# Kernel optimization log

Hardware: AMD Instinct MI355X
Metric: run time of the kernel (lower is better)

Reference implementation:

```python
import jax, jax.numpy as jnp
import numpy as np

S = 1        # support_num
K = 20       # neighbor_num for conv stages
EPS_BN = 1e-5

def _normalize(x, axis):
    n = jnp.linalg.norm(x, axis=axis, keepdims=True)
    return x / jnp.maximum(n, 1e-12)

def _knn(verts, k):
    # verts: (b, v, 3) -> (b, v, k) nearest-neighbor indices excluding self
    sq = jnp.sum(verts * verts, axis=-1)                                   # (b, v)
    d = sq[:, :, None] + sq[:, None, :] - 2.0 * jnp.einsum('bic,bjc->bij', verts, verts)
    _, idx = jax.lax.top_k(-d, k + 1)                                      # smallest distances
    return idx[:, :, 1:]

def _gather(t, idx):
    # t: (b, v, c), idx: (b, v, n) -> (b, v, n, c)
    return jax.vmap(lambda tb, ib: tb[ib])(t, idx)

def _theta(nidx, verts, directions, out_c):
    # relu(cos angle) between normalized neighbor directions and support directions
    ndir = _normalize(_gather(verts, nidx) - verts[:, :, None, :], -1)     # (b, v, n, 3)
    sdir = _normalize(directions, 0)                                       # (3, S*out_c)
    th = jax.nn.relu(jnp.einsum('bvnc,ck->bvnk', ndir, sdir))
    b, v, n, _ = th.shape
    return th.reshape(b, v, n, S, out_c)

def _conv_surface(nidx, verts, directions, kernel_num):
    th = _theta(nidx, verts, directions, kernel_num)                       # (b,v,n,S,k)
    return th.max(axis=2).sum(axis=2)                                      # (b, v, k)

def _conv_layer(nidx, verts, fm, w, bias, directions, out_c):
    th = _theta(nidx, verts, directions, out_c)                            # (b,v,n,S,o)
    fout = fm @ w + bias                                                   # (b,v,(S+1)*o)
    center = fout[..., :out_c]
    support = _gather(fout[..., out_c:], nidx)                             # (b,v,n,S*o)
    b, v, n, _ = support.shape
    act = (th * support.reshape(b, v, n, S, out_c)).max(axis=2).sum(axis=2)
    return center + act

def _bn(x):
    # BatchNorm1d(affine=False) training-mode: per-channel over (batch, vertices)
    m = jnp.mean(x, axis=(0, 1))
    v = jnp.var(x, axis=(0, 1))
    return (x - m) * jax.lax.rsqrt(v + EPS_BN)

def _pool(verts, fm, rate, nk):
    nidx = _knn(verts, nk)
    pooled = _gather(fm, nidx).max(axis=2)
    pn = verts.shape[1] // rate
    # deterministic subsample (original uses randperm; fixed choice for a stable baseline)
    return verts[:, :pn], pooled[:, :pn]

def _forward(vertices, c0_dir, c1_w, c1_b, c1_dir, d1_w, c2_w, c2_b, c2_dir, d2_w,
             c3_w, c3_b, c3_dir, d3_w, c4_w, c4_b, c4_dir, d4_w,
             cls_w1, cls_b1, cls_g, cls_beta, cls_w2, cls_b2):
    verts = jnp.transpose(vertices, (0, 2, 1))                             # (b, N, 3)
    nidx = _knn(verts, K)
    fm0 = jax.nn.relu(_conv_surface(nidx, verts, c0_dir, 32))
    res1 = fm0 @ d1_w.T
    fm1 = jax.nn.relu(_bn(_conv_layer(nidx, verts, fm0, c1_w, c1_b, c1_dir, 64))) + res1
    verts, fm1 = _pool(verts, fm1, 4, 4)
    nidx = _knn(verts, K)
    res2 = fm1 @ d2_w.T
    fm2 = jax.nn.relu(_bn(_conv_layer(nidx, verts, fm1, c2_w, c2_b, c2_dir, 128))) + res2
    res3 = fm2 @ d3_w.T
    fm3 = jax.nn.relu(_bn(_conv_layer(nidx, verts, fm2, c3_w, c3_b, c3_dir, 256))) + res3
    verts, fm3 = _pool(verts, fm3, 4, 4)
    nidx = _knn(verts, K)
    res4 = fm3 @ d4_w.T
    fm4 = jax.nn.relu(_bn(_conv_layer(nidx, verts, fm3, c4_w, c4_b, c4_dir, 1024))) + res4
    g = fm4.max(axis=1)                                                    # (b, 1024)
    h = g @ cls_w1.T + cls_b1
    m = jnp.mean(h, axis=0); var = jnp.var(h, axis=0)                      # BN(256), dropout=eval identity
    h = (h - m) * jax.lax.rsqrt(var + EPS_BN) * cls_g + cls_beta
    h = jax.nn.relu(h)
    return h @ cls_w2.T + cls_b2                                           # (b, 40)

def setup_inputs() -> dict:
    key = jax.random.key(0)
    ks = jax.random.split(key, 24)
    def u(k, shape, s=0.05):
        return jax.random.uniform(k, shape, jnp.float32, -s, s)
    return {
        'vertices': jax.random.normal(ks[0], (32, 3, 1024), jnp.float32),
        'c0_dir': u(ks[1], (3, S * 32)),
        'c1_w': u(ks[2], (32, (S + 1) * 64)),  'c1_b': u(ks[3], ((S + 1) * 64,)),  'c1_dir': u(ks[4], (3, S * 64)),
        'd1_w': u(ks[5], (64, 32)),
        'c2_w': u(ks[6], (64, (S + 1) * 128)), 'c2_b': u(ks[7], ((S + 1) * 128,)), 'c2_dir': u(ks[8], (3, S * 128)),
        'd2_w': u(ks[9], (128, 64)),
        'c3_w': u(ks[10], (128, (S + 1) * 256)), 'c3_b': u(ks[11], ((S + 1) * 256,)), 'c3_dir': u(ks[12], (3, S * 256)),
        'd3_w': u(ks[13], (256, 128)),
        'c4_w': u(ks[14], (256, (S + 1) * 1024)), 'c4_b': u(ks[15], ((S + 1) * 1024,)), 'c4_dir': u(ks[16], (3, S * 1024)),
        'd4_w': u(ks[17], (1024, 256)),
        'cls_w1': u(ks[18], (256, 1024)), 'cls_b1': u(ks[19], (256,)),
        'cls_g': jnp.ones((256,), jnp.float32), 'cls_beta': jnp.zeros((256,), jnp.float32),
        'cls_w2': u(ks[20], (40, 256)), 'cls_b2': u(ks[21], (40,)),
    }

def reference(vertices, c0_dir, c1_w, c1_b, c1_dir, d1_w, c2_w, c2_b, c2_dir, d2_w,
              c3_w, c3_b, c3_dir, d3_w, c4_w, c4_b, c4_dir, d4_w,
              cls_w1, cls_b1, cls_g, cls_beta, cls_w2, cls_b2):
    return _forward(vertices, c0_dir, c1_w, c1_b, c1_dir, d1_w, c2_w, c2_b, c2_dir, d2_w,
                    c3_w, c3_b, c3_dir, d3_w, c4_w, c4_b, c4_dir, d4_w,
                    cls_w1, cls_b1, cls_g, cls_beta, cls_w2, cls_b2)
```

## Files before the change

### kernel.cpp

```cpp
#include <hip/hip_runtime.h>

#define TPB 256
#define KNN_TPB 512
static inline int nblk(long n) { return (int)((n + TPB - 1) / TPB); }

#define FINF 3.402823466e38f

template <int NS, bool WDIR, bool CSURF, int K2>
__device__ __forceinline__ void knn_body(int bx, int b, const float* __restrict__ vin,
                                         int* __restrict__ knn, float* __restrict__ ndir,
                                         int V_out, const float* __restrict__ c0dir,
                                         float* __restrict__ fm0, int V2, int* __restrict__ knn4,
                                         float4* pts, int (*sidx)[20], float (*sdir)[20][3],
                                         unsigned (*cdist)[256], unsigned short (*cidx)[256]) {
    constexpr int K = 20;
    constexpr int VF = NS * 64;
    const float* vb = vin + (size_t)b * 3072;
    for (int j = threadIdx.x; j < VF; j += blockDim.x) {
        float x = vb[j], y = vb[1024 + j], z = vb[2048 + j];
        pts[j] = make_float4(x, y, z, x * x + y * y + z * z);
    }
    __syncthreads();
    int lane = threadIdx.x & 63;
    int w = threadIdx.x >> 6;
    int i = bx * 8 + w;
    if (i >= V_out) return;
    float4 pi = pts[i];
    unsigned ud[NS];
    unsigned lmin = 0xFFFFFFFFu;
#pragma unroll
    for (int s = 0; s < NS; ++s) {
        int j = s * 64 + lane;
        float4 pj = pts[j];
        float dist = pi.w + pj.w - 2.f * (pi.x * pj.x + pi.y * pj.y + pi.z * pj.z);
        dist = fmaxf(dist, 0.f);
        unsigned v = (j == i) ? 0xFFFFFFFFu : __float_as_uint(dist);
        ud[s] = v;
        lmin = v < lmin ? v : lmin;
    }
    unsigned pmin = lmin;
    {
        unsigned o = (unsigned)__shfl_xor((int)pmin, 1, 64);
        pmin = o < pmin ? o : pmin;
    }
    unsigned gmin = lmin, M = pmin;
#pragma unroll
    for (int off = 32; off > 1; off >>= 1) {
        unsigned on = (unsigned)__shfl_xor((int)gmin, off, 64);
        gmin = on < gmin ? on : gmin;
        unsigned om = (unsigned)__shfl_xor((int)M, off, 64);
        M = om > M ? om : M;
    }
    {
        unsigned on = (unsigned)__shfl_xor((int)gmin, 1, 64);
        gmin = on < gmin ? on : gmin;
    }
    int* orow = knn + ((size_t)(b * V_out + i)) * K;
    unsigned long long lmask = (1ull << lane) - 1ull;
    bool done = false;
    if constexpr (NS >= 8) {
        int cnt = 0;
#pragma unroll
        for (int s = 0; s < NS; ++s) {
            unsigned long long mm = __ballot(ud[s] <= M);
            if (ud[s] <= M) {
                int p = cnt + __popcll(mm & lmask);
                if (p < 256) { cdist[w][p] = ud[s]; cidx[w][p] = (unsigned short)(s * 64 + lane); }
            }
            cnt += __popcll(mm);
        }
        if (cnt <= 256) {
            unsigned cd[4];
#pragma unroll
            for (int r = 0; r < 4; ++r) {
                int p = lane + r * 64;
                cd[r] = p < cnt ? cdist[w][p] : 0xFFFFFFFFu;
            }
            unsigned lo = gmin, hi = M + 1u;
            while (hi - lo > 1u) {
                unsigned mid = lo + ((hi - lo) >> 1);
                int c = 0;
#pragma unroll
                for (int r = 0; r < 4; ++r)
                    c += __popcll(__ballot(cd[r] < mid));
                if (c >= K) hi = mid; else lo = mid;
            }
            unsigned T = lo;
            int base = 0;
#pragma unroll
            for (int r = 0; r < 4; ++r) {
                unsigned long long mm = __ballot(cd[r] < T);
                if (cd[r] < T) {
                    int p = base + __popcll(mm & lmask);
                    int j = cidx[w][lane + r * 64];
                    sidx[w][p] = j; orow[p] = j;
                }
                base += __popcll(mm);
            }
            int need = K - base, run = 0;
#pragma unroll
            for (int r = 0; r < 4; ++r) {
                unsigned long long mm = __ballot(cd[r] == T);
                int rr = run + __popcll(mm & lmask);
                if (cd[r] == T && rr < need) {
                    int j = cidx[w][lane + r * 64];
                    sidx[w][base + rr] = j; orow[base + rr] = j;
                }
                run += __popcll(mm);
            }
            done = true;
        }
    }
    if (!done) {
        unsigned lo = gmin, hi = M + 1u;
        while (hi - lo > 1u) {
            unsigned mid = lo + ((hi - lo) >> 1);
            int cnt = 0;
#pragma unroll
            for (int s = 0; s < NS; ++s)
                cnt += __popcll(__ballot(ud[s] < mid));
            if (cnt >= K) hi = mid; else lo = mid;
        }
        unsigned T = lo;
        int base = 0;
#pragma unroll
        for (int s = 0; s < NS; ++s) {
            unsigned long long m = __ballot(ud[s] < T);
            if (ud[s] < T) {
                int p = base + __popcll(m & lmask);
                sidx[w][p] = s * 64 + lane;
                orow[p] = s * 64 + lane;
            }
            base += __popcll(m);
        }
        int need = K - base, run = 0;
#pragma unroll
        for (int s = 0; s < NS; ++s) {
            unsigned long long m = __ballot(ud[s] == T);
            int r = run + __popcll(m & lmask);
            if (ud[s] == T && r < need) {
                sidx[w][base + r] = s * 64 + lane;
                orow[base + r] = s * 64 + lane;
            }
            run += __popcll(m);
        }
    }
    if (WDIR) {
        if (lane < K) {
            int j = sidx[w][lane];
            float4 pj = pts[j];
            float dx = pj.x - pi.x, dy = pj.y - pi.y, dz = pj.z - pi.z;
            float inv = 1.f / fmaxf(sqrtf(dx * dx + dy * dy + dz * dz), 1e-12f);
            float* o = ndir + ((size_t)(b * V_out + i) * K + lane) * 3;
            float nx = dx * inv, ny = dy * inv, nz = dz * inv;
            o[0] = nx; o[1] = ny; o[2] = nz;
            if (CSURF) { sdir[w][lane][0] = nx; sdir[w][lane][1] = ny; sdir[w][lane][2] = nz; }
        }
        if (CSURF && lane < 32) {
            int c = lane;
            float d0 = c0dir[c], d1 = c0dir[32 + c], d2 = c0dir[64 + c];
            float inv = 1.f / fmaxf(sqrtf(d0 * d0 + d1 * d1 + d2 * d2), 1e-12f);
            d0 *= inv; d1 *= inv; d2 *= inv;
            float m = 0.f;
            for (int n = 0; n < K; ++n) {
                float th = sdir[w][n][0] * d0 + sdir[w][n][1] * d1 + sdir[w][n][2] * d2;
                m = fmaxf(m, th);
            }
            fm0[(size_t)(b * V_out + i) * 32 + c] = m;
        }
    }
    if (K2 > 0 && i < V2) {
        float dsel = FINF;
        int jsel = 0x7FFFFFFF;
        if (lane < K) {
            jsel = sidx[w][lane];
            float4 pj = pts[jsel];
            dsel = fmaxf(pi.w + pj.w - 2.f * (pi.x * pj.x + pi.y * pj.y + pi.z * pj.z), 0.f);
        }
        int rank = 0;
        for (int m = 0; m < K; ++m) {
            float dm = __shfl(dsel, m, 64);
            int jm = __shfl(jsel, m, 64);
            rank += (dm < dsel || (dm == dsel && jm < jsel)) ? 1 : 0;
        }
        if (lane < K && rank < K2) knn4[((size_t)(b * V2 + i)) * K2 + rank] = jsel;
    }
}

__global__ __launch_bounds__(KNN_TPB, 1) void prep_kernel(const float* __restrict__ vin, const float* __restrict__ c0dir,
                                                          int* __restrict__ knn1, float* __restrict__ ndir1,
                                                          float* __restrict__ fm0, int* __restrict__ knn4_1,
                                                          int* __restrict__ knn2, float* __restrict__ ndir2,
                                                          int* __restrict__ knn4_2,
                                                          int* __restrict__ knn3, float* __restrict__ ndir3,
                                                          const float* __restrict__ d1, const float* __restrict__ d2,
                                                          const float* __restrict__ d3, const float* __restrict__ d4,
                                                          float* __restrict__ o1, float* __restrict__ o2,
                                                          float* __restrict__ o3, float* __restrict__ o4,
                                                          float* __restrict__ pz) {
    __shared__ float4 pts[1024];
    __shared__ int sidx[8][20];
    __shared__ float sdir[8][20][3];
    __shared__ unsigned cdist[8][256];
    __shared__ unsigned short cidx[8][256];
    int bx = blockIdx.x, b = blockIdx.y;
    if (bx < 128) {
        knn_body<16, true, true, 4>(bx, b, vin, knn1, ndir1, 1024, c0dir, fm0, 256, knn4_1,
                                    pts, sidx, sdir, cdist, cidx);
        return;
    }
    if (bx < 160) {
        knn_body<4, true, false, 4>(bx - 128, b, vin, knn2, ndir2, 256, nullptr, nullptr, 64, knn4_2,
                                    pts, sidx, sdir, cdist, cidx);
        return;
    }
    if (bx < 168) {
        knn_body<1, true, false, 0>(bx - 160, b, vin, knn3, ndir3, 64, nullptr, nullptr, 0, nullptr,
                                    pts, sidx, sdir, cdist, cidx);
        return;
    }
    if (b != 0) return;
    if (bx < 764) {
        int t = (bx - 168) * KNN_TPB + threadIdx.x;
        if (t < 2048) { int r = t / 32, c = t % 32; o1[c * 64 + r] = d1[t]; return; }
        int t2 = t - 2048;
        if (t2 < 8192) { int r = t2 / 64, c = t2 % 64; o2[c * 128 + r] = d2[t2]; return; }
        int t3 = t2 - 8192;
        if (t3 < 32768) { int r = t3 / 128, c = t3 % 128; o3[c * 256 + r] = d3[t3]; return; }
        int t4 = t3 - 32768;
        if (t4 < 262144) { int r = t4 / 256, c = t4 % 256; o4[c * 1024 + r] = d4[t4]; }
        return;
    }
    int t5 = (bx - 764) * KNN_TPB + threadIdx.x;
    if (t5 < 57344) pz[t5] = 0.f;
}

template <int MODE>
__global__ __launch_bounds__(TPB) void gemm64_kernel(const float* __restrict__ A, const float* __restrict__ W,
                                                     const float* __restrict__ bias,
                                                     const float* __restrict__ conv, const float* __restrict__ partial,
                                                     float* __restrict__ out, int M, int N, int K, int nsplit) {
    __shared__ float As[64][36];
    __shared__ float Bs[32][68];
    __shared__ float smean[64], sinv[64];
    int t = threadIdx.x;
    int tx = t & 15, ty = t >> 4;
    int colbase = blockIdx.x * 64, rowbase = blockIdx.y * 64;
    int r0 = ty * 4, c0 = tx * 4;
    if constexpr (MODE >= 1) {
        __shared__ double sred[2][4][64];
        int cc = t & 63, g = t >> 6;
        double s = 0.0, ss = 0.0;
        for (int sp = g; sp < nsplit; sp += 4) {
            s += partial[(size_t)sp * 2 * N + colbase + cc];
            ss += partial[(size_t)sp * 2 * N + N + colbase + cc];
        }
        sred[0][g][cc] = s; sred[1][g][cc] = ss;
        __syncthreads();
        if (t < 64) {
            double S = sred[0][0][t] + sred[0][1][t] + sred[0][2][t] + sred[0][3][t];
            double SS = sred[1][0][t] + sred[1][1][t] + sred[1][2][t] + sred[1][3][t];
            double mean = S / M;
            double var = SS / M - mean * mean;
            if (var < 0) var = 0;
            smean[t] = (float)mean;
            sinv[t] = rsqrtf((float)var + 1e-5f);
        }
        __syncthreads();
    }
    float4 acc0, acc1, acc2, acc3;
    if (MODE == 0) {
        float4 bv = *(const float4*)(bias + colbase + c0);
        acc0 = bv; acc1 = bv; acc2 = bv; acc3 = bv;
    } else {
        acc0 = make_float4(0.f, 0.f, 0.f, 0.f); acc1 = acc0; acc2 = acc0; acc3 = acc0;
    }
    for (int kt = 0; kt < K; kt += 32) {
#pragma unroll
        for (int l = 0; l < 2; ++l) {
            int lin = t + l * 256;
            int ar = lin >> 3, ak = (lin & 7) << 2;
            *(float4*)&As[ar][ak] = *(const float4*)(A + (size_t)(rowbase + ar) * K + kt + ak);
            int br = lin >> 4, bn = (lin & 15) << 2;
            *(float4*)&Bs[br][bn] = *(const float4*)(W + (size_t)(kt + br) * N + colbase + bn);
        }
        __syncthreads();
#pragma unroll 4
        for (int k = 0; k < 32; ++k) {
            float4 bv = *(const float4*)&Bs[k][c0];
            float a0 = As[r0][k], a1 = As[r0 + 1][k], a2 = As[r0 + 2][k], a3 = As[r0 + 3][k];
            acc0.x += a0 * bv.x; acc0.y += a0 * bv.y; acc0.z += a0 * bv.z; acc0.w += a0 * bv.w;
            acc1.x += a1 * bv.x; acc1.y += a1 * bv.y; acc1.z += a1 * bv.z; acc1.w += a1 * bv.w;
            acc2.x += a2 * bv.x; acc2.y += a2 * bv.y; acc2.z += a2 * bv.z; acc2.w += a2 * bv.w;
            acc3.x += a3 * bv.x; acc3.y += a3 * bv.y; acc3.z += a3 * bv.z; acc3.w += a3 * bv.w;
        }
        __syncthreads();
    }
    float4 accs[4] = {acc0, acc1, acc2, acc3};
    if constexpr (MODE >= 1) {
        float4 mean = *(const float4*)&smean[c0];
        float4 inv = *(const float4*)&sinv[c0];
#pragma unroll
        for (int rr = 0; rr < 4; ++rr) {
            float4 cv = *(const float4*)(conv + (size_t)(rowbase + r0 + rr) * N + colbase + c0);
            accs[rr].x += fmaxf((cv.x - mean.x) * inv.x, 0.f);
            accs[rr].y += fmaxf((cv.y - mean.y) * inv.y, 0.f);
            accs[rr].z += fmaxf((cv.z - mean.z) * inv.z, 0.f);
            accs[rr].w += fmaxf((cv.w - mean.w) * inv.w, 0.f);
        }
    }
    if constexpr (MODE == 2) {
        __shared__ float redmax[16][68];
        float4 tm;
        tm.x = fmaxf(fmaxf(accs[0].x, accs[1].x), fmaxf(accs[2].x, accs[3].x));
        tm.y = fmaxf(fmaxf(accs[0].y, accs[1].y), fmaxf(accs[2].y, accs[3].y));
        tm.z = fmaxf(fmaxf(accs[0].z, accs[1].z), fmaxf(accs[2].z, accs[3].z));
        tm.w = fmaxf(fmaxf(accs[0].w, accs[1].w), fmaxf(accs[2].w, accs[3].w));
        *(float4*)&redmax[ty][c0] = tm;
        __syncthreads();
        if (t < 64) {
            float m = redmax[0][t];
#pragma unroll
            for (int g = 1; g < 16; ++g) m = fmaxf(m, redmax[g][t]);
            out[(size_t)blockIdx.y * N + colbase + t] = m;
        }
    } else {
#pragma unroll
        for (int rr = 0; rr < 4; ++rr)
            *(float4*)(out + (size_t)(rowbase + r0 + rr) * N + colbase + c0) = accs[rr];
    }
}

template <bool FUSE>
__global__ __launch_bounds__(TPB) void conv_act_kernel(const float* __restrict__ ndir, const int* __restrict__ knn,
                                const float* __restrict__ fout, const float* __restrict__ dir,
                                float* __restrict__ out, int B, int Vst, int K, int Cout,
                                float* __restrict__ bnpart) {
    __shared__ float sAcc[2][256];
    int t = blockIdx.x * blockDim.x + threadIdx.x;
    int nc4 = Cout >> 2;
    bool active = t < B * Vst * nc4;
    float4 o = make_float4(0.f, 0.f, 0.f, 0.f);
    int c4 = 0;
    if (active) {
        int row = t / nc4; c4 = (t % nc4) * 4;
        int b = row / Vst;
        float4 D0 = *(const float4*)(dir + c4);
        float4 D1 = *(const float4*)(dir + Cout + c4);
        float4 D2 = *(const float4*)(dir + 2 * Cout + c4);
        float4 e0, e1, e2;
        {
            float i0 = 1.f / fmaxf(sqrtf(D0.x * D0.x + D1.x * D1.x + D2.x * D2.x), 1e-12f);
            float i1 = 1.f / fmaxf(sqrtf(D0.y * D0.y + D1.y * D1.y + D2.y * D2.y), 1e-12f);
            float i2 = 1.f / fmaxf(sqrtf(D0.z * D0.z + D1.z * D1.z + D2.z * D2.z), 1e-12f);
            float i3 = 1.f / fmaxf(sqrtf(D0.w * D0.w + D1.w * D1.w + D2.w * D2.w), 1e-12f);
            e0 = make_float4(D0.x * i0, D0.y * i1, D0.z * i2, D0.w * i3);
            e1 = make_float4(D1.x * i0, D1.y * i1, D1.z * i2, D1.w * i3);
            e2 = make_float4(D2.x * i0, D2.y * i1, D2.z * i2, D2.w * i3);
        }
        int Cw = 2 * Cout;
        float4 m = make_float4(-FINF, -FINF, -FINF, -FINF);
        const float* nd = ndir + (size_t)row * K * 3;
        const int* kr = knn + (size_t)row * K;
        for (int n = 0; n < K; ++n) {
            int j = kr[n];
            float n0 = nd[n * 3], n1 = nd[n * 3 + 1], n2 = nd[n * 3 + 2];
            float4 s = *(const float4*)(fout + ((size_t)(b * Vst + j)) * Cw + Cout + c4);
            float t0 = fmaxf(n0 * e0.x + n1 * e1.x + n2 * e2.x, 0.f);
            float t1 = fmaxf(n0 * e0.y + n1 * e1.y + n2 * e2.y, 0.f);
            float t2 = fmaxf(n0 * e0.z + n1 * e1.z + n2 * e2.z, 0.f);
            float t3 = fmaxf(n0 * e0.w + n1 * e1.w + n2 * e2.w, 0.f);
            m.x = fmaxf(m.x, t0 * s.x);
            m.y = fmaxf(m.y, t1 * s.y);
            m.z = fmaxf(m.z, t2 * s.z);
            m.w = fmaxf(m.w, t3 * s.w);
        }
        float4 ctr = *(const float4*)(fout + (size_t)row * Cw + c4);
        o = make_float4(ctr.x + m.x, ctr.y + m.y, ctr.z + m.z, ctr.w + m.w);
        *(float4*)(out + (size_t)row * Cout + c4) = o;
    }
    if constexpr (FUSE) {
        for (int i = threadIdx.x; i < 2 * Cout; i += TPB) ((float*)sAcc)[i < Cout ? i : 256 + (i - Cout)] = 0.f;
        __syncthreads();
        if (active) {
            atomicAdd(&sAcc[0][c4 + 0], o.x); atomicAdd(&sAcc[1][c4 + 0], o.x * o.x);
            atomicAdd(&sAcc[0][c4 + 1], o.y); atomicAdd(&sAcc[1][c4 + 1], o.y * o.y);
            atomicAdd(&sAcc[0][c4 + 2], o.z); atomicAdd(&sAcc[1][c4 + 2], o.z * o.z);
            atomicAdd(&sAcc[0][c4 + 3], o.w); atomicAdd(&sAcc[1][c4 + 3], o.w * o.w);
        }
        __syncthreads();
        int bin = blockIdx.x & 63;
        for (int i = threadIdx.x; i < Cout; i += TPB) {
            atomicAdd(&bnpart[(size_t)bin * 2 * Cout + i], sAcc[0][i]);
            atomicAdd(&bnpart[(size_t)bin * 2 * Cout + Cout + i], sAcc[1][i]);
        }
    }
}

__global__ __launch_bounds__(TPB) void conv_act_s3_kernel(const float* __restrict__ ndir, const int* __restrict__ knn,
                                                          const float* __restrict__ fout, const float* __restrict__ dir,
                                                          float* __restrict__ out, float* __restrict__ bnpart) {
    constexpr int Cout = 1024, K = 20, Vst = 64, Cw = 2048;
    __shared__ float sred[2][4][256];
    int bid = blockIdx.x;
    int rg = bid >> 2, cslice = bid & 3;
    int rowlane = threadIdx.x >> 6;
    int lc4 = threadIdx.x & 63;
    int c4 = cslice * 256 + lc4 * 4;
    float4 D0 = *(const float4*)(dir + c4);
    float4 D1 = *(const float4*)(dir + Cout + c4);
    float4 D2 = *(const float4*)(dir + 2 * Cout + c4);
    float4 e0, e1, e2;
    {
        float i0 = 1.f / fmaxf(sqrtf(D0.x * D0.x + D1.x * D1.x + D2.x * D2.x), 1e-12f);
        float i1 = 1.f / fmaxf(sqrtf(D0.y * D0.y + D1.y * D1.y + D2.y * D2.y), 1e-12f);
        float i2 = 1.f / fmaxf(sqrtf(D0.z * D0.z + D1.z * D1.z + D2.z * D2.z), 1e-12f);
        float i3 = 1.f / fmaxf(sqrtf(D0.w * D0.w + D1.w * D1.w + D2.w * D2.w), 1e-12f);
        e0 = make_float4(D0.x * i0, D0.y * i1, D0.z * i2, D0.w * i3);
        e1 = make_float4(D1.x * i0, D1.y * i1, D1.z * i2, D1.w * i3);
        e2 = make_float4(D2.x * i0, D2.y * i1, D2.z * i2, D2.w * i3);
    }
    float4 sum = make_float4(0.f, 0.f, 0.f, 0.f);
    float4 ssum = make_float4(0.f, 0.f, 0.f, 0.f);
#pragma unroll
    for (int it = 0; it < 4; ++it) {
        int row = rg * 16 + it * 4 + rowlane;
        int b = row >> 6;
        float4 m = make_float4(-FINF, -FINF, -FINF, -FINF);
        const float* nd = ndir + (size_t)row * K * 3;
        const int* kr = knn + (size_t)row * K;
        for (int n = 0; n < K; ++n) {
            int j = kr[n];
            float n0 = nd[n * 3], n1 = nd[n * 3 + 1], n2 = nd[n * 3 + 2];
            float4 s = *(const float4*)(fout + ((size_t)(b * Vst + j)) * Cw + Cout + c4);
            float t0 = fmaxf(n0 * e0.x + n1 * e1.x + n2 * e2.x, 0.f);
            float t1 = fmaxf(n0 * e0.y + n1 * e1.y + n2 * e2.y, 0.f);
            float t2 = fmaxf(n0 * e0.z + n1 * e1.z + n2 * e2.z, 0.f);
            float t3 = fmaxf(n0 * e0.w + n1 * e1.w + n2 * e2.w, 0.f);
            m.x = fmaxf(m.x, t0 * s.x);
            m.y = fmaxf(m.y, t1 * s.y);
            m.z = fmaxf(m.z, t2 * s.z);
            m.w = fmaxf(m.w, t3 * s.w);
        }
        float4 ctr = *(const float4*)(fout + (size_t)row * Cw + c4);
        float4 o = make_float4(ctr.x + m.x, ctr.y + m.y, ctr.z + m.z, ctr.w + m.w);
        *(float4*)(out + (size_t)row * Cout + c4) = o;
        sum.x += o.x; sum.y += o.y; sum.z += o.z; sum.w += o.w;
        ssum.x += o.x * o.x; ssum.y += o.y * o.y; ssum.z += o.z * o.z; ssum.w += o.w * o.w;
    }
    *(float4*)&sred[0][rowlane][lc4 * 4] = sum;
    *(float4*)&sred[1][rowlane][lc4 * 4] = ssum;
    __syncthreads();
    int c = threadIdx.x;
    float S = sred[0][0][c] + sred[0][1][c] + sred[0][2][c] + sred[0][3][c];
    float SS = sred[1][0][c] + sred[1][1][c] + sred[1][2][c] + sred[1][3][c];
    bnpart[(size_t)rg * 2048 + cslice * 256 + c] = S;
    bnpart[(size_t)rg * 2048 + 1024 + cslice * 256 + c] = SS;
}

__global__ __launch_bounds__(TPB) void pool_max_kernel(const float* __restrict__ fm, const int* __restrict__ knn4,
                                float* __restrict__ out, int B, int Vin, int pn, int C) {
    int t = blockIdx.x * blockDim.x + threadIdx.x;
    if (t >= B * pn * C) return;
    int row = t / C, c = t % C;
    int b = row / pn;
    const int* kr = knn4 + (size_t)row * 4;
    float m = fmaxf(fmaxf(fm[((size_t)(b * Vin + kr[0])) * C + c], fm[((size_t)(b * Vin + kr[1])) * C + c]),
                    fmaxf(fm[((size_t)(b * Vin + kr[2])) * C + c], fm[((size_t)(b * Vin + kr[3])) * C + c]));
    out[t] = m;
}

__global__ __launch_bounds__(TPB, 1) void gemm_t_wave_kernel(const float* __restrict__ in, const float* __restrict__ w,
                                   const float* __restrict__ bias, float* __restrict__ out,
                                   int rows, int Cin, int Cout) {
    int wid = (blockIdx.x * blockDim.x + threadIdx.x) >> 6;
    int lane = threadIdx.x & 63;
    if (wid >= rows * Cout) return;
    int r = wid / Cout, c = wid % Cout;
    const float4* a = (const float4*)(in + (size_t)r * Cin);
    const float4* wr = (const float4*)(w + (size_t)c * Cin);
    int n4 = Cin >> 2;
    float acc = 0.f;
    for (int k = lane; k < n4; k += 64) {
        float4 av = a[k], wv = wr[k];
        acc += av.x * wv.x + av.y * wv.y + av.z * wv.z + av.w * wv.w;
    }
#pragma unroll
    for (int off = 32; off > 0; off >>= 1) acc += __shfl_xor(acc, off, 64);
    if (lane == 0) out[wid] = acc + bias[c];
}

__global__ __launch_bounds__(TPB, 1) void cls_fused_kernel(const float* __restrict__ h,
                                 const float* __restrict__ gam, const float* __restrict__ beta,
                                 const float* __restrict__ w2, const float* __restrict__ b2,
                                 float* __restrict__ out) {
    __shared__ float smean[256], sa[256];
    int t = threadIdx.x;
    {
        float s = 0.f, ss = 0.f;
        for (int b = 0; b < 32; ++b) {
            float v = h[(size_t)b * 256 + t];
            s += v; ss += v * v;
        }
        float mn = s / 32.f;
        float var = ss / 32.f - mn * mn;
        if (var < 0.f) var = 0.f;
        smean[t] = mn;
        sa[t] = rsqrtf(var + 1e-5f) * gam[t];
    }
    __syncthreads();
    int wid = blockIdx.x * 4 + (t >> 6);
    int lane = t & 63;
    if (wid >= 32 * 40) return;
    int b = wid / 40, o = wid % 40;
    float acc = 0.f;
#pragma unroll
    for (int kk = 0; kk < 4; ++kk) {
        int c = lane + kk * 64;
        float v = fmaxf((h[b * 256 + c] - smean[c]) * sa[c] + beta[c], 0.f);
        acc += v * w2[o * 256 + c];
    }
#pragma unroll
    for (int off = 32; off > 0; off >>= 1) acc += __shfl_xor(acc, off, 64);
    if (lane == 0) out[wid] = acc + b2[o];
}

extern "C" void kernel_launch(void* const* d_in, const int* in_sizes, int n_in,
                              void* d_out, int out_size, void* d_ws, size_t ws_size,
                              hipStream_t stream) {
    const float* vertices = (const float*)d_in[0];
    const float* c0_dir = (const float*)d_in[1];
    const float* c1_w  = (const float*)d_in[2];
    const float* c1_b  = (const float*)d_in[3];
    const float* c1_dir = (const float*)d_in[4];
    const float* d1_w  = (const float*)d_in[5];
    const float* c2_w  = (const float*)d_in[6];
    const float* c2_b  = (const float*)d_in[7];
    const float* c2_dir = (const float*)d_in[8];
    const float* d2_w  = (const float*)d_in[9];
    const float* c3_w  = (const float*)d_in[10];
    const float* c3_b  = (const float*)d_in[11];
    const float* c3_dir = (const float*)d_in[12];
    const float* d3_w  = (const float*)d_in[13];
    const float* c4_w  = (const float*)d_in[14];
    const float* c4_b  = (const float*)d_in[15];
    const float* c4_dir = (const float*)d_in[16];
    const float* d4_w  = (const float*)d_in[17];
    const float* cls_w1 = (const float*)d_in[18];
    const float* cls_b1 = (const float*)d_in[19];
    const float* cls_g  = (const float*)d_in[20];
    const float* cls_beta = (const float*)d_in[21];
    const float* cls_w2 = (const float*)d_in[22];
    const float* cls_b2 = (const float*)d_in[23];

    const int B = 32;
    float* ws = (float*)d_ws;
    size_t off = 0;
    auto alloc = [&](size_t n) { float* p = ws + off; off += n; return p; };
    int*   knn1  = (int*)alloc(655360);
    int*   knn2  = (int*)alloc(163840);
    int*   knn3  = (int*)alloc(40960);
    int*   knn4_1 = (int*)alloc(32768);
    int*   knn4_2 = (int*)alloc(8192);
    float* ndir1 = alloc(1966080);
    float* ndir2 = alloc(491520);
    float* ndir3 = alloc(122880);
    float* fm0   = alloc(1048576);
    float* fm1   = alloc(2097152);
    float* fm1p  = alloc(524288);
    float* fm2   = alloc(1048576);
    float* fm3   = alloc(2097152);
    float* fm3p  = alloc(524288);
    float* fout  = alloc(4194304);
    float* convp = alloc(2097152);
    float* gbuf  = alloc(32768);
    float* hbuf  = alloc(8192);
    float* d1t   = alloc(2048);
    float* d2t   = alloc(8192);
    float* d3t   = alloc(32768);
    float* d4t   = alloc(262144);
    float* pz    = alloc(57344);
    float* p1    = pz;
    float* p2a   = pz + 8192;
    float* p2b   = pz + 24576;
    float* p3    = alloc(262144);

    prep_kernel<<<dim3(876, B), KNN_TPB, 0, stream>>>(
        vertices, c0_dir, knn1, ndir1, fm0, knn4_1, knn2, ndir2, knn4_2, knn3, ndir3,
        d1_w, d2_w, d3_w, d4_w, d1t, d2t, d3t, d4t, pz);

    gemm64_kernel<0><<<dim3(2, 512), TPB, 0, stream>>>(fm0, c1_w, c1_b, nullptr, nullptr, fout, B * 1024, 128, 32, 0);
    conv_act_kernel<true><<<nblk((long)B * 1024 * 16), TPB, 0, stream>>>(ndir1, knn1, fout, c1_dir, convp, B, 1024, 20, 64, p1);
    gemm64_kernel<1><<<dim3(1, 512), TPB, 0, stream>>>(fm0, d1t, nullptr, convp, p1, fm1, B * 1024, 64, 32, 64);
    pool_max_kernel<<<nblk((long)B * 256 * 64), TPB, 0, stream>>>(fm1, knn4_1, fm1p, B, 1024, 256, 64);

    gemm64_kernel<0><<<dim3(4, 128), TPB, 0, stream>>>(fm1p, c2_w, c2_b, nullptr, nullptr, fout, B * 256, 256, 64, 0);
    conv_act_kernel<true><<<nblk((long)B * 256 * 32), TPB, 0, stream>>>(ndir2, knn2, fout, c2_dir, convp, B, 256, 20, 128, p2a);
    gemm64_kernel<1><<<dim3(2, 128), TPB, 0, stream>>>(fm1p, d2t, nullptr, convp, p2a, fm2, B * 256, 128, 64, 64);
    gemm64_kernel<0><<<dim3(8, 128), TPB, 0, stream>>>(fm2, c3_w, c3_b, nullptr, nullptr, fout, B * 256, 512, 128, 0);
    conv_act_kernel<true><<<nblk((long)B * 256 * 64), TPB, 0, stream>>>(ndir2, knn2, fout, c3_dir, convp, B, 256, 20, 256, p2b);
    gemm64_kernel<1><<<dim3(4, 128), TPB, 0, stream>>>(fm2, d3t, nullptr, convp, p2b, fm3, B * 256, 256, 128, 64);
    pool_max_kernel<<<nblk((long)B * 64 * 256), TPB, 0, stream>>>(fm3, knn4_2, fm3p, B, 256, 64, 256);

    gemm64_kernel<0><<<dim3(32, 32), TPB, 0, stream>>>(fm3p, c4_w, c4_b, nullptr, nullptr, fout, B * 64, 2048, 256, 0);
    conv_act_s3_kernel<<<512, TPB, 0, stream>>>(ndir3, knn3, fout, c4_dir, convp, p3);
    gemm64_kernel<2><<<dim3(16, 32), TPB, 0, stream>>>(fm3p, d4t, nullptr, convp, p3, gbuf, B * 64, 1024, 256, 128);

    gemm_t_wave_kernel<<<nblk((long)32 * 256 * 64), TPB, 0, stream>>>(gbuf, cls_w1, cls_b1, hbuf, 32, 1024, 256);
    cls_fused_kernel<<<320, TPB, 0, stream>>>(hbuf, cls_g, cls_beta, cls_w2, cls_b2, (float*)d_out);
}
```

Before: 344.6 us.

## Fuse stage-4 conv GEMM with neighbor max-activation and BN partial sums

Replaces the separate stage-4 GEMM and conv_act_s3 kernels with one kernel. Each block computes the center and support GEMM tiles for one batch's 64 vertices, keeps the support tile in shared memory, and gathers neighbors from it instead of from global fout. This removes the 2048-wide fout write and its re-read plus one launch. BN partials are now reduced per batch, so the partial count argument changes from 128 to 32. The cost is more shared memory per block and a larger GEMM body with fewer blocks.

```diff
diff --git a/kernel.cpp b/kernel.cpp
--- a/kernel.cpp
+++ b/kernel.cpp
@@ -397,19 +397,65 @@
     }
 }
 
-__global__ __launch_bounds__(TPB) void conv_act_s3_kernel(const float* __restrict__ ndir, const int* __restrict__ knn,
-                                                          const float* __restrict__ fout, const float* __restrict__ dir,
-                                                          float* __restrict__ out, float* __restrict__ bnpart) {
-    constexpr int Cout = 1024, K = 20, Vst = 64, Cw = 2048;
-    __shared__ float sred[2][4][256];
-    int bid = blockIdx.x;
-    int rg = bid >> 2, cslice = bid & 3;
-    int rowlane = threadIdx.x >> 6;
-    int lc4 = threadIdx.x & 63;
-    int c4 = cslice * 256 + lc4 * 4;
-    float4 D0 = *(const float4*)(dir + c4);
-    float4 D1 = *(const float4*)(dir + Cout + c4);
-    float4 D2 = *(const float4*)(dir + 2 * Cout + c4);
+__global__ __launch_bounds__(TPB) void s3_fused_kernel(const float* __restrict__ A, const float* __restrict__ W,
+                                                       const float* __restrict__ bias,
+                                                       const float* __restrict__ ndir, const int* __restrict__ knn,
+                                                       const float* __restrict__ dir,
+                                                       float* __restrict__ convp, float* __restrict__ bnpart) {
+    constexpr int K = 256, N = 2048, Cout = 1024, KN = 20;
+    __shared__ float As[64][36];
+    __shared__ float Bc[32][68];
+    __shared__ float Bsup[32][68];
+    __shared__ float S[64][68];
+    __shared__ float red[2][16][68];
+    int t = threadIdx.x;
+    int tx = t & 15, ty = t >> 4;
+    int r0 = ty * 4, c0 = tx * 4;
+    int batch = blockIdx.y;
+    int colbase = blockIdx.x * 64;
+    int rowbase = batch * 64;
+    float4 accC[4], accS[4];
+    {
+        float4 bc = *(const float4*)(bias + colbase + c0);
+        float4 bs = *(const float4*)(bias + Cout + colbase + c0);
+#pragma unroll
+        for (int rr = 0; rr < 4; ++rr) { accC[rr] = bc; accS[rr] = bs; }
+    }
+    for (int kt = 0; kt < K; kt += 32) {
+#pragma unroll
+        for (int l = 0; l < 2; ++l) {
+            int lin = t + l * 256;
+            int ar = lin >> 3, ak = (lin & 7) << 2;
+            *(float4*)&As[ar][ak] = *(const float4*)(A + (size_t)(rowbase + ar) * K + kt + ak);
+            int br = lin >> 4, bn = (lin & 15) << 2;
+            *(float4*)&Bc[br][bn] = *(const float4*)(W + (size_t)(kt + br) * N + colbase + bn);
+            *(float4*)&Bsup[br][bn] = *(const float4*)(W + (size_t)(kt + br) * N + Cout + colbase + bn);
+        }
+        __syncthreads();
+#pragma unroll 4
+        for (int k = 0; k < 32; ++k) {
+            float4 bc = *(const float4*)&Bc[k][c0];
+            float4 bs = *(const float4*)&Bsup[k][c0];
+            float a0 = As[r0][k], a1 = As[r0 + 1][k], a2 = As[r0 + 2][k], a3 = As[r0 + 3][k];
+            accC[0].x += a0 * bc.x; accC[0].y += a0 * bc.y; accC[0].z += a0 * bc.z; accC[0].w += a0 * bc.w;
+            accC[1].x += a1 * bc.x; accC[1].y += a1 * bc.y; accC[1].z += a1 * bc.z; accC[1].w += a1 * bc.w;
+            accC[2].x += a2 * bc.x; accC[2].y += a2 * bc.y; accC[2].z += a2 * bc.z; accC[2].w += a2 * bc.w;
+            accC[3].x += a3 * bc.x; accC[3].y += a3 * bc.y; accC[3].z += a3 * bc.z; accC[3].w += a3 * bc.w;
+            accS[0].x += a0 * bs.x; accS[0].y += a0 * bs.y; accS[0].z += a0 * bs.z; accS[0].w += a0 * bs.w;
+            accS[1].x += a1 * bs.x; accS[1].y += a1 * bs.y; accS[1].z += a1 * bs.z; accS[1].w += a1 * bs.w;
+            accS[2].x += a2 * bs.x; accS[2].y += a2 * bs.y; accS[2].z += a2 * bs.z; accS[2].w += a2 * bs.w;
+            accS[3].x += a3 * bs.x; accS[3].y += a3 * bs.y; accS[3].z += a3 * bs.z; accS[3].w += a3 * bs.w;
+        }
+        __syncthreads();
+    }
+#pragma unroll
+    for (int rr = 0; rr < 4; ++rr)
+        *(float4*)&S[r0 + rr][c0] = accS[rr];
+    __syncthreads();
+    int c = colbase + c0;
+    float4 D0 = *(const float4*)(dir + c);
+    float4 D1 = *(const float4*)(dir + Cout + c);
+    float4 D2 = *(const float4*)(dir + 2 * Cout + c);
     float4 e0, e1, e2;
     {
         float i0 = 1.f / fmaxf(sqrtf(D0.x * D0.x + D1.x * D1.x + D2.x * D2.x), 1e-12f);
@@ -423,16 +469,15 @@
     float4 sum = make_float4(0.f, 0.f, 0.f, 0.f);
     float4 ssum = make_float4(0.f, 0.f, 0.f, 0.f);
 #pragma unroll
-    for (int it = 0; it < 4; ++it) {
-        int row = rg * 16 + it * 4 + rowlane;
-        int b = row >> 6;
+    for (int rr = 0; rr < 4; ++rr) {
+        int row = rowbase + r0 + rr;
         float4 m = make_float4(-FINF, -FINF, -FINF, -FINF);
-        const float* nd = ndir + (size_t)row * K * 3;
-        const int* kr = knn + (size_t)row * K;
-        for (int n = 0; n < K; ++n) {
+        const float* nd = ndir + (size_t)row * KN * 3;
+        const int* kr = knn + (size_t)row * KN;
+        for (int n = 0; n < KN; ++n) {
             int j = kr[n];
             float n0 = nd[n * 3], n1 = nd[n * 3 + 1], n2 = nd[n * 3 + 2];
-            float4 s = *(const float4*)(fout + ((size_t)(b * Vst + j)) * Cw + Cout + c4);
+            float4 s = *(const float4*)&S[j][c0];
             float t0 = fmaxf(n0 * e0.x + n1 * e1.x + n2 * e2.x, 0.f);
             float t1 = fmaxf(n0 * e0.y + n1 * e1.y + n2 * e2.y, 0.f);
             float t2 = fmaxf(n0 * e0.z + n1 * e1.z + n2 * e2.z, 0.f);
@@ -442,20 +487,21 @@
             m.z = fmaxf(m.z, t2 * s.z);
             m.w = fmaxf(m.w, t3 * s.w);
         }
-        float4 ctr = *(const float4*)(fout + (size_t)row * Cw + c4);
-        float4 o = make_float4(ctr.x + m.x, ctr.y + m.y, ctr.z + m.z, ctr.w + m.w);
-        *(float4*)(out + (size_t)row * Cout + c4) = o;
+        float4 o = make_float4(accC[rr].x + m.x, accC[rr].y + m.y, accC[rr].z + m.z, accC[rr].w + m.w);
+        *(float4*)(convp + (size_t)row * Cout + colbase + c0) = o;
         sum.x += o.x; sum.y += o.y; sum.z += o.z; sum.w += o.w;
         ssum.x += o.x * o.x; ssum.y += o.y * o.y; ssum.z += o.z * o.z; ssum.w += o.w * o.w;
     }
-    *(float4*)&sred[0][rowlane][lc4 * 4] = sum;
-    *(float4*)&sred[1][rowlane][lc4 * 4] = ssum;
+    *(float4*)&red[0][ty][c0] = sum;
+    *(float4*)&red[1][ty][c0] = ssum;
     __syncthreads();
-    int c = threadIdx.x;
-    float S = sred[0][0][c] + sred[0][1][c] + sred[0][2][c] + sred[0][3][c];
-    float SS = sred[1][0][c] + sred[1][1][c] + sred[1][2][c] + sred[1][3][c];
-    bnpart[(size_t)rg * 2048 + cslice * 256 + c] = S;
-    bnpart[(size_t)rg * 2048 + 1024 + cslice * 256 + c] = SS;
+    if (t < 64) {
+        float Ssum = 0.f, SSsum = 0.f;
+#pragma unroll
+        for (int g = 0; g < 16; ++g) { Ssum += red[0][g][t]; SSsum += red[1][g][t]; }
+        bnpart[(size_t)batch * 2048 + colbase + t] = Ssum;
+        bnpart[(size_t)batch * 2048 + 1024 + colbase + t] = SSsum;
+    }
 }
 
 __global__ __launch_bounds__(TPB) void pool_max_kernel(const float* __restrict__ fm, const int* __restrict__ knn4,
@@ -583,7 +629,7 @@
     float* p1    = pz;
     float* p2a   = pz + 8192;
     float* p2b   = pz + 24576;
-    float* p3    = alloc(262144);
+    float* p3    = alloc(65536);
 
     prep_kernel<<<dim3(876, B), KNN_TPB, 0, stream>>>(
         vertices, c0_dir, knn1, ndir1, fm0, knn4_1, knn2, ndir2, knn4_2, knn3, ndir3,
@@ -602,9 +648,8 @@
     gemm64_kernel<1><<<dim3(4, 128), TPB, 0, stream>>>(fm2, d3t, nullptr, convp, p2b, fm3, B * 256, 256, 128, 64);
     pool_max_kernel<<<nblk((long)B * 64 * 256), TPB, 0, stream>>>(fm3, knn4_2, fm3p, B, 256, 64, 256);
 
-    gemm64_kernel<0><<<dim3(32, 32), TPB, 0, stream>>>(fm3p, c4_w, c4_b, nullptr, nullptr, fout, B * 64, 2048, 256, 0);
-    conv_act_s3_kernel<<<512, TPB, 0, stream>>>(ndir3, knn3, fout, c4_dir, convp, p3);
-    gemm64_kernel<2><<<dim3(16, 32), TPB, 0, stream>>>(fm3p, d4t, nullptr, convp, p3, gbuf, B * 64, 1024, 256, 128);
+    s3_fused_kernel<<<dim3(16, 32), TPB, 0, stream>>>(fm3p, c4_w, c4_b, ndir3, knn3, c4_dir, convp, p3);
+    gemm64_kernel<2><<<dim3(16, 32), TPB, 0, stream>>>(fm3p, d4t, nullptr, convp, p3, gbuf, B * 64, 1024, 256, 32);
 
     gemm_t_wave_kernel<<<nblk((long)32 * 256 * 64), TPB, 0, stream>>>(gbuf, cls_w1, cls_b1, hbuf, 32, 1024, 256);
     cls_fused_kernel<<<320, TPB, 0, stream>>>(hbuf, cls_g, cls_beta, cls_w2, cls_b2, (float*)d_out);
```

Result: faster. 320.0 us (median of 3 runs) (-7.1%).
